# Kernel tuning notes

Measured on AMD Instinct MI355X. Metric: run time of the kernel, lower is better.

Reference implementation:

```python
import jax, jax.numpy as jnp
import numpy as np

N_EMBD = 1024
N_HEAD = 16
HEAD_DIM = N_EMBD // N_HEAD

def setup_inputs() -> dict:
    key = jax.random.key(0)
    ks = jax.random.split(key, 5)
    B, T, C = 2, 2048, N_EMBD
    s = 1.0 / np.sqrt(C)
    x = jax.random.normal(ks[0], (B, T, C), dtype=jnp.float32)
    W_qkv = jax.random.normal(ks[1], (C, 3 * C), dtype=jnp.float32) * s
    b_qkv = jax.random.normal(ks[2], (3 * C,), dtype=jnp.float32) * 0.02
    W_o = jax.random.normal(ks[3], (C, C), dtype=jnp.float32) * s
    b_o = jax.random.normal(ks[4], (C,), dtype=jnp.float32) * 0.02
    return {"x": x, "W_qkv": W_qkv, "b_qkv": b_qkv, "W_o": W_o, "b_o": b_o}

def reference(x, W_qkv, b_qkv, W_o, b_o):
    B, T, C = x.shape
    H, D = N_HEAD, HEAD_DIM
    scale = 1.0 / np.sqrt(D)
    qkv = jnp.einsum('btc,cf->btf', x, W_qkv) + b_qkv  # [B,T,3C]
    q, k, v = jnp.split(qkv, 3, axis=-1)
    # [B,H,T,D]
    q = q.reshape(B, T, H, D).transpose(0, 2, 1, 3)
    k = k.reshape(B, T, H, D).transpose(0, 2, 1, 3)
    v = v.reshape(B, T, H, D).transpose(0, 2, 1, 3)
    att = jnp.einsum('bhqd,bhkd->bhqk', q, k) * scale  # [B,H,T,T]
    causal = jnp.tril(jnp.ones((T, T), dtype=bool))
    att = jnp.where(causal[None, None], att, -jnp.inf)
    att = jax.nn.softmax(att, axis=-1)
    y = jnp.einsum('bhqk,bhkd->bhqd', att, v)  # [B,H,T,D]
    y = y.transpose(0, 2, 1, 3).reshape(B, T, C)
    return jnp.einsum('btc,cf->btf', y, W_o) + b_o
```

## Files before the change

kernel.cpp:

```cpp
#include <hip/hip_runtime.h>
#include <hip/hip_bf16.h>

#define TT 2048
#define BB 2
#define CC 1024
#define NH 16
#define HD 64

typedef __attribute__((ext_vector_type(8))) short short8;
typedef __attribute__((ext_vector_type(4))) short short4b;
typedef __attribute__((ext_vector_type(4))) float f32x4;

typedef unsigned int __attribute__((address_space(1))) ui_gas;
typedef unsigned int __attribute__((address_space(3))) ui_las;

#if __has_builtin(__builtin_amdgcn_mfma_f32_16x16x16bf16_1k)
#define PV16 1
#define VSS 4
#else
#define PV16 0
#define VSS 8
#endif

__device__ __forceinline__ float us2f(unsigned short u) {
    union { unsigned int i; float f; } v; v.i = ((unsigned int)u) << 16; return v.f;
}
__device__ __forceinline__ unsigned short f2us(float f) {
    union { float f; unsigned int i; } v; v.f = f;
    unsigned int i = v.i;
    unsigned int lsb = (i >> 16) & 1u;
    i += 0x7fffu + lsb;
    return (unsigned short)(i >> 16);
}
__device__ __forceinline__ unsigned int pack2_trunc(float a, float b) {
    union { float f; unsigned int u; } x, y; x.f = a; y.f = b;
    return (y.u & 0xffff0000u) | (x.u >> 16);
}

__device__ __forceinline__ void gl_lds16(const unsigned short* g, unsigned short* l) {
    __builtin_amdgcn_global_load_lds((const ui_gas*)g, (ui_las*)l, 16, 0, 0);
}

__device__ __forceinline__ float4 load4(const void* p, size_t i, int isbf) {
    if (isbf) {
        ushort4 u = *reinterpret_cast<const ushort4*>((const unsigned short*)p + i);
        return make_float4(us2f(u.x), us2f(u.y), us2f(u.z), us2f(u.w));
    } else {
        return *reinterpret_cast<const float4*>((const float*)p + i);
    }
}
__device__ __forceinline__ float load1(const void* p, size_t i, int isbf) {
    return isbf ? us2f(((const unsigned short*)p)[i]) : ((const float*)p)[i];
}

__global__ __launch_bounds__(256) void prep_kernel(
    const void* __restrict__ x, const void* __restrict__ Wqkv, const void* __restrict__ Wo,
    const void* __restrict__ bqkv, const void* __restrict__ bo,
    unsigned short* __restrict__ xb, unsigned short* __restrict__ Wqkvt,
    unsigned short* __restrict__ Wot, int* __restrict__ flags)
{
    __shared__ float Ls[64 * 65];
    __shared__ int sh_isbf;
    const int t = threadIdx.x;
    const int bid = blockIdx.x;

    const void* src;
    int mode, sub;
    if (bid < 2048)      { mode = 0; sub = bid;        src = x; }
    else if (bid < 2816) { mode = 1; sub = bid - 2048; src = Wqkv; }
    else                 { mode = 2; sub = bid - 2816; src = Wo; }

    if (bid == 0 && t < 64) {
        const void* ps[5] = {x, Wqkv, bqkv, Wo, bo};
        for (int k = 0; k < 5; ++k) {
            const unsigned short* u = (const unsigned short*)ps[k];
            int bad = 0;
            #pragma unroll
            for (int j = 0; j < 4; ++j) {
                float v = us2f(u[t * 4 + j]);
                if (!(fabsf(v) < 1e4f)) bad = 1;
            }
            unsigned long long m = __ballot(bad != 0);
            if (t == 0) flags[k] = (__popcll(m) < 4) ? 1 : 0;
        }
    }
    if (t < 64) {
        const unsigned short* u = (const unsigned short*)src;
        int bad = 0;
        #pragma unroll
        for (int j = 0; j < 4; ++j) {
            float v = us2f(u[t * 4 + j]);
            if (!(fabsf(v) < 1e4f)) bad = 1;
        }
        unsigned long long m = __ballot(bad != 0);
        if (t == 0) sh_isbf = (__popcll(m) < 4) ? 1 : 0;
    }
    __syncthreads();
    const int isbf = sh_isbf;

    if (mode == 0) {
        const size_t i = ((size_t)sub * 256 + t) * 8;
        float4 a = load4(src, i, isbf);
        float4 b = load4(src, i + 4, isbf);
        alignas(16) unsigned short pk[8];
        pk[0] = f2us(a.x); pk[1] = f2us(a.y); pk[2] = f2us(a.z); pk[3] = f2us(a.w);
        pk[4] = f2us(b.x); pk[5] = f2us(b.y); pk[6] = f2us(b.z); pk[7] = f2us(b.w);
        *reinterpret_cast<uint4*>(xb + i) = *reinterpret_cast<const uint4*>(pk);
        return;
    }

    int N, Krows, n0, k0;
    unsigned short* dst;
    if (mode == 1) { N = 3 * CC; Krows = CC; dst = Wqkvt; n0 = (sub % 48) * 64; k0 = (sub / 48) * 64; }
    else           { N = CC;     Krows = CC; dst = Wot;   n0 = (sub % 16) * 64; k0 = (sub / 16) * 64; }
    {
        const int r = t >> 2, cq = (t & 3) << 4;
        #pragma unroll
        for (int i = 0; i < 4; ++i) {
            float4 v = load4(src, (size_t)(k0 + r) * N + n0 + cq + i * 4, isbf);
            Ls[r * 65 + cq + i * 4 + 0] = v.x;
            Ls[r * 65 + cq + i * 4 + 1] = v.y;
            Ls[r * 65 + cq + i * 4 + 2] = v.z;
            Ls[r * 65 + cq + i * 4 + 3] = v.w;
        }
    }
    __syncthreads();
    {
        const int c = t & 63, kg = (t >> 6) * 16;
        alignas(16) unsigned short pk[16];
        #pragma unroll
        for (int i = 0; i < 16; ++i) pk[i] = f2us(Ls[(kg + i) * 65 + c]);
        unsigned short* d = dst + (size_t)(n0 + c) * Krows + k0 + kg;
        *reinterpret_cast<uint4*>(d + 0) = *reinterpret_cast<const uint4*>(&pk[0]);
        *reinterpret_cast<uint4*>(d + 8) = *reinterpret_cast<const uint4*>(&pk[8]);
    }
}

template<int WM, int WN, int NWM, int NWN>
__global__ __launch_bounds__(256) void gemm_mfma(
    const unsigned short* __restrict__ A,
    const unsigned short* __restrict__ Bt,
    const void* __restrict__ bias, void* __restrict__ C,
    unsigned short* __restrict__ Vt,
    int M, int N, int K,
    const int* __restrict__ flags, int biasfi, int cfi)
{
    constexpr int BM = WM * 16 * NWM, BN = WN * 16 * NWN;
    constexpr int ASL = BM / 16, BSL = BN / 16;

    const int bias_bf = (biasfi >= 0) ? flags[biasfi] : 0;
    const int c_bf    = (cfi >= 0) ? flags[cfi] : ((cfi == -2) ? 1 : 0);

    __shared__ __align__(16) unsigned short Asl[2][ASL * 2 * 512];
    __shared__ __align__(16) unsigned short Bsl[2][BSL * 2 * 512];

    const int tid = threadIdx.x;
    const int l  = tid & 63;
    const int w  = tid >> 6;
    const int wm = w / NWN, wn = w % NWN;
    const int bm = blockIdx.y * BM, bn = blockIdx.x * BN;
    const int lm = l & 15;
    const int lk = (l >> 4) * 8;

    f32x4 acc[WM][WN];
    #pragma unroll
    for (int i = 0; i < WM; ++i)
        #pragma unroll
        for (int j = 0; j < WN; ++j) acc[i][j] = (f32x4){0.f, 0.f, 0.f, 0.f};

    auto stage = [&](int bb, int k0) {
        #pragma unroll
        for (int s = 0; s < ASL / 4; ++s) {
            const int r = w * (ASL / 4) + s;
            #pragma unroll
            for (int kh = 0; kh < 2; ++kh)
                gl_lds16(A + (size_t)(bm + r * 16 + lm) * K + k0 + kh * 32 + lk,
                         &Asl[bb][(r * 2 + kh) * 512]);
        }
        #pragma unroll
        for (int s = 0; s < BSL / 4; ++s) {
            const int r = w * (BSL / 4) + s;
            #pragma unroll
            for (int kh = 0; kh < 2; ++kh)
                gl_lds16(Bt + (size_t)(bn + r * 16 + lm) * K + k0 + kh * 32 + lk,
                         &Bsl[bb][(r * 2 + kh) * 512]);
        }
    };

    auto compute = [&](int bb) {
        #pragma unroll
        for (int kh = 0; kh < 2; ++kh) {
            short8 af[WM], bf[WN];
            #pragma unroll
            for (int i = 0; i < WM; ++i)
                af[i] = *reinterpret_cast<const short8*>(&Asl[bb][((WM * wm + i) * 2 + kh) * 512 + l * 8]);
            #pragma unroll
            for (int j = 0; j < WN; ++j)
                bf[j] = *reinterpret_cast<const short8*>(&Bsl[bb][((WN * wn + j) * 2 + kh) * 512 + l * 8]);
            #pragma unroll
            for (int i = 0; i < WM; ++i)
                #pragma unroll
                for (int j = 0; j < WN; ++j)
                    acc[i][j] = __builtin_amdgcn_mfma_f32_16x16x32_bf16(af[i], bf[j], acc[i][j], 0, 0, 0);
        }
    };

    stage(0, 0);
    __syncthreads();
    const int nt = K >> 6;
    for (int t = 0; t < nt; ++t) {
        if (t + 1 < nt) stage((t + 1) & 1, (t + 1) << 6);
        compute(t & 1);
        __syncthreads();
    }

    const int quad = l >> 4;
    float bv[WN];
    #pragma unroll
    for (int j = 0; j < WN; ++j) bv[j] = load1(bias, bn + (WN * wn + j) * 16 + lm, bias_bf);

    #pragma unroll
    for (int i = 0; i < WM; ++i) {
        #pragma unroll
        for (int r = 0; r < 4; ++r) {
            const int row = bm + (WM * wm + i) * 16 + quad * 4 + r;
            #pragma unroll
            for (int j = 0; j < WN; ++j) {
                const int col = bn + (WN * wn + j) * 16 + lm;
                const float val = acc[i][j][r] + bv[j];
                if (c_bf) {
                    const unsigned short us = f2us(val);
                    ((unsigned short*)C)[(size_t)row * N + col] = us;
                    if (Vt != nullptr && col >= 2 * CC) {
                        const int cc2 = col - 2 * CC;
                        const int h = cc2 >> 6, d = cc2 & 63;
                        const int bq = row / TT, tk = row % TT;
                        Vt[((size_t)(bq * NH + h) * HD + d) * TT + tk] = us;
                    }
                } else {
                    ((float*)C)[(size_t)row * N + col] = val;
                }
            }
        }
    }
}

__global__ __launch_bounds__(256) void attn_mfma(
    const unsigned short* __restrict__ qkv,
    const unsigned short* __restrict__ Vt,
    unsigned short* __restrict__ y)
{
    __shared__ __align__(16) unsigned short Ksh[2][8 * 512];
    __shared__ __align__(16) unsigned short Vsh[2][1039 * VSS];

    const int tid = threadIdx.x;
    const int l   = tid & 63;
    const int w   = tid >> 6;
    const int quad = l >> 4;
    const int col  = l & 15;

    const int n  = blockIdx.x;
    const int g  = n >> 3;
    const int bh = (n & 7) * 4 + (g & 3);
    const int i  = g >> 2;
    const int tA = i, tB = 31 - i;
    const int b  = bh >> 4, h = bh & 15;

#if !PV16
    {
        unsigned short* vflat = &Vsh[0][0];
        for (int ss = tid; ss < 1039 * 2; ss += 256)
            *(uint2*)(&vflat[ss * 8 + 4]) = make_uint2(0u, 0u);
    }
#endif

    const float QSCALE = 0.18033688f;
    short8 qfA[2], qfB[2];
    #pragma unroll
    for (int t2 = 0; t2 < 2; ++t2) {
        const int qt = t2 ? tB : tA;
        short8* qf = t2 ? qfB : qfA;
        const int token = qt * 64 + w * 16 + col;
        const unsigned short* qrow = qkv + (size_t)(b * TT + token) * 3 * CC + h * HD;
        #pragma unroll
        for (int ks = 0; ks < 2; ++ks) {
            ushort4 u0 = *(const ushort4*)(qrow + ks * 32 + quad * 8);
            ushort4 u1 = *(const ushort4*)(qrow + ks * 32 + quad * 8 + 4);
            alignas(16) unsigned short pk[8];
            pk[0] = f2us(us2f(u0.x) * QSCALE);
            pk[1] = f2us(us2f(u0.y) * QSCALE);
            pk[2] = f2us(us2f(u0.z) * QSCALE);
            pk[3] = f2us(us2f(u0.w) * QSCALE);
            pk[4] = f2us(us2f(u1.x) * QSCALE);
            pk[5] = f2us(us2f(u1.y) * QSCALE);
            pk[6] = f2us(us2f(u1.z) * QSCALE);
            pk[7] = f2us(us2f(u1.w) * QSCALE);
            qf[ks] = *(const short8*)pk;
        }
    }

    f32x4 oA[4], oB[4];
    #pragma unroll
    for (int nb = 0; nb < 4; ++nb) {
        oA[nb] = (f32x4){0.f, 0.f, 0.f, 0.f};
        oB[nb] = (f32x4){0.f, 0.f, 0.f, 0.f};
    }
    float lAc = 0.f, lBc = 0.f;

    const unsigned short* kbase = qkv + (size_t)b * TT * 3 * CC + CC + h * HD;
    const unsigned short* vbase = Vt + (size_t)bh * HD * TT;

    const int vd = tid >> 2, vg0 = (tid & 3) * 4;

    uint4 rk[2], rv[2];
    auto issue_loads = [&](int kt) {
        const unsigned short* ksrc = kbase + (size_t)(kt * 64 + l) * 3 * CC;
        #pragma unroll
        for (int c2 = 0; c2 < 2; ++c2) {
            const int c = 2 * w + c2;
            rk[c2] = *(const uint4*)(ksrc + c * 8);
        }
        const unsigned short* vsrc = vbase + (size_t)vd * TT + kt * 64 + vg0 * 4;
        rv[0] = *(const uint4*)(vsrc + 0);
        rv[1] = *(const uint4*)(vsrc + 8);
    };
    auto write_lds = [&](int bb) {
        #pragma unroll
        for (int c2 = 0; c2 < 2; ++c2) {
            const int c = 2 * w + c2;
            const int ks = c >> 2, q = c & 3;
            const int slot = ((quad * 2 + ks) * 64 + q * 16 + col) * 8;
            *(uint4*)(&Ksh[bb][slot]) = rk[c2];
        }
        *(uint2*)(&Vsh[bb][((vg0 + 0) * 65 + vd) * VSS]) = make_uint2(rv[0].x, rv[0].y);
        *(uint2*)(&Vsh[bb][((vg0 + 1) * 65 + vd) * VSS]) = make_uint2(rv[0].z, rv[0].w);
        *(uint2*)(&Vsh[bb][((vg0 + 2) * 65 + vd) * VSS]) = make_uint2(rv[1].x, rv[1].y);
        *(uint2*)(&Vsh[bb][((vg0 + 3) * 65 + vd) * VSS]) = make_uint2(rv[1].z, rv[1].w);
    };

    auto step = [&](const short8* qf, f32x4* o, float& l_i, bool diag, int bb) {
        f32x4 st[4];
        __builtin_amdgcn_s_setprio(1);
        #pragma unroll
        for (int nb = 0; nb < 4; ++nb) {
            f32x4 acc = {0.f, 0.f, 0.f, 0.f};
            #pragma unroll
            for (int ks = 0; ks < 2; ++ks) {
                short8 kf = *(const short8*)(&Ksh[bb][((nb * 2 + ks) * 64 + l) * 8]);
                acc = __builtin_amdgcn_mfma_f32_16x16x32_bf16(kf, qf[ks], acc, 0, 0, 0);
            }
            st[nb] = acc;
        }
        __builtin_amdgcn_s_setprio(0);
        float pv[4][4];
        float rs = 0.f;
        #pragma unroll
        for (int nb = 0; nb < 4; ++nb)
            #pragma unroll
            for (int r = 0; r < 4; ++r) {
                float v = st[nb][r];
                if (diag && (nb * 16 + quad * 4 + r > w * 16 + col)) v = -3e38f;
                float p = __builtin_exp2f(v);
                pv[nb][r] = p;
                rs += p;
            }
        rs += __shfl_xor(rs, 16);
        rs += __shfl_xor(rs, 32);
        l_i += rs;
#if PV16
        short4b pf[4];
        #pragma unroll
        for (int nbk = 0; nbk < 4; ++nbk) {
            union { short4b s; unsigned int u[2]; } pk;
            pk.u[0] = pack2_trunc(pv[nbk][0], pv[nbk][1]);
            pk.u[1] = pack2_trunc(pv[nbk][2], pv[nbk][3]);
            pf[nbk] = pk.s;
        }
        __builtin_amdgcn_s_setprio(1);
        #pragma unroll
        for (int nbd = 0; nbd < 4; ++nbd)
            #pragma unroll
            for (int nbk = 0; nbk < 4; ++nbk) {
                short4b vf = *(const short4b*)(&Vsh[bb][((nbk * 4 + quad) * 65 + nbd * 16 + col) * VSS]);
                o[nbd] = __builtin_amdgcn_mfma_f32_16x16x16bf16_1k(pf[nbk], vf, o[nbd], 0, 0, 0);
            }
        __builtin_amdgcn_s_setprio(0);
#else
        short8 pf[4];
        #pragma unroll
        for (int nbk = 0; nbk < 4; ++nbk) {
            union { short8 s; unsigned int u[4]; } pk;
            pk.u[0] = pack2_trunc(pv[nbk][0], pv[nbk][1]);
            pk.u[1] = pack2_trunc(pv[nbk][2], pv[nbk][3]);
            pk.u[2] = 0u; pk.u[3] = 0u;
            pf[nbk] = pk.s;
        }
        __builtin_amdgcn_s_setprio(1);
        #pragma unroll
        for (int nbd = 0; nbd < 4; ++nbd)
            #pragma unroll
            for (int nbk = 0; nbk < 4; ++nbk) {
                short8 vf = *(const short8*)(&Vsh[bb][((nbk * 4 + quad) * 65 + nbd * 16 + col) * VSS]);
                o[nbd] = __builtin_amdgcn_mfma_f32_16x16x32_bf16(pf[nbk], vf, o[nbd], 0, 0, 0);
            }
        __builtin_amdgcn_s_setprio(0);
#endif
    };

    issue_loads(0);
    write_lds(0);
    __syncthreads();
    for (int kt = 0; kt <= tB; ++kt) {
        const int cur = kt & 1;
        if (kt < tB) issue_loads(kt + 1);
        step(qfB, oB, lBc, kt == tB, cur);
        if (kt <= tA) step(qfA, oA, lAc, kt == tA, cur);
        if (kt < tB) write_lds(cur ^ 1);
        __syncthreads();
    }

    #pragma unroll
    for (int t2 = 0; t2 < 2; ++t2) {
        const int qt = t2 ? tB : tA;
        f32x4* o = t2 ? oB : oA;
        const float inv = 1.f / (t2 ? lBc : lAc);
        float invr[4];
        #pragma unroll
        for (int r = 0; r < 4; ++r) invr[r] = __shfl(inv, quad * 4 + r);
        #pragma unroll
        for (int nb = 0; nb < 4; ++nb)
            #pragma unroll
            for (int r = 0; r < 4; ++r) {
                int token = qt * 64 + w * 16 + quad * 4 + r;
                y[(size_t)(b * TT + token) * CC + h * HD + nb * 16 + col] = f2us(o[nb][r] * invr[r]);
            }
    }
}

extern "C" void kernel_launch(void* const* d_in, const int* in_sizes, int n_in,
                              void* d_out, int out_size, void* d_ws, size_t ws_size,
                              hipStream_t stream) {
    const int M = BB * TT;

    char* ws = (char*)d_ws;
    int*            flags = (int*)ws;                         ws += 256;
    unsigned short* xb    = (unsigned short*)ws;              ws += (size_t)M * CC * 2;
    unsigned short* Wqkvt = (unsigned short*)ws;              ws += (size_t)3 * CC * CC * 2;
    unsigned short* Wot   = (unsigned short*)ws;              ws += (size_t)CC * CC * 2;
    unsigned short* qkv   = (unsigned short*)ws;              ws += (size_t)M * 3 * CC * 2;
    unsigned short* Vt    = (unsigned short*)ws;              ws += (size_t)BB * NH * HD * TT * 2;
    unsigned short* y     = (unsigned short*)ws;

    prep_kernel<<<3072, 256, 0, stream>>>(d_in[0], d_in[1], d_in[3], d_in[2], d_in[4],
                                          xb, Wqkvt, Wot, flags);

    gemm_mfma<4, 4, 2, 2><<<dim3(3 * CC / 128, M / 128), 256, 0, stream>>>(
        xb, Wqkvt, d_in[2], qkv, Vt, M, 3 * CC, CC, flags, 2, -2);

    attn_mfma<<<512, 256, 0, stream>>>(qkv, Vt, y);

    gemm_mfma<2, 4, 4, 1><<<dim3(CC / 64, M / 128), 256, 0, stream>>>(
        y, Wot, d_in[4], d_out, nullptr, M, CC, CC, flags, 4, 0);
}
```

Measured before the change: 249.3 us.

## Replace LDS-staged GEMMs with register-direct global loads and XCD-aware block swizzle

Both projection GEMMs drop the shared-memory double-buffered staging and barriers. Each wave now loads its MFMA fragments straight from global memory into registers, double-buffered across 32-wide K steps with the K loop fully unrolled. Block indices are remapped so blocks landing on the same XCD cover neighbouring tiles, which is meant to improve L2 reuse, and the QKV GEMM tile shape changes to 256x64. This removes LDS traffic and sync overhead, but each wave now reads its own A/B data with no sharing inside the block, so global and L2 traffic rises and register pressure grows.

```diff
diff --git a/kernel.cpp b/kernel.cpp
--- a/kernel.cpp
+++ b/kernel.cpp
@@ -35,10 +35,6 @@
 __device__ __forceinline__ unsigned int pack2_trunc(float a, float b) {
     union { float f; unsigned int u; } x, y; x.f = a; y.f = b;
     return (y.u & 0xffff0000u) | (x.u >> 16);
-}
-
-__device__ __forceinline__ void gl_lds16(const unsigned short* g, unsigned short* l) {
-    __builtin_amdgcn_global_load_lds((const ui_gas*)g, (ui_las*)l, 16, 0, 0);
 }
 
 __device__ __forceinline__ float4 load4(const void* p, size_t i, int isbf) {
@@ -136,106 +132,105 @@
     }
 }
 
-template<int WM, int WN, int NWM, int NWN>
-__global__ __launch_bounds__(256) void gemm_mfma(
+template<int WM, int WN, int KC, int SWZ, bool VTE>
+__global__ __launch_bounds__(256) void gemm_reg(
     const unsigned short* __restrict__ A,
     const unsigned short* __restrict__ Bt,
     const void* __restrict__ bias, void* __restrict__ C,
     unsigned short* __restrict__ Vt,
-    int M, int N, int K,
+    int M, int N,
     const int* __restrict__ flags, int biasfi, int cfi)
 {
-    constexpr int BM = WM * 16 * NWM, BN = WN * 16 * NWN;
-    constexpr int ASL = BM / 16, BSL = BN / 16;
+    constexpr int HS = KC / 32;
+    const int tid = threadIdx.x;
+    const int l   = tid & 63;
+    const int w   = tid >> 6;
+    const int lm  = l & 15;
+    const int lk  = (l >> 4) * 8;
+    const int quad = l >> 4;
+
+    int bx, by;
+    if constexpr (SWZ == 1) {
+        const int lin = blockIdx.y * 48 + blockIdx.x;
+        const int xcd = lin & 7, loc = lin >> 3;
+        bx = (xcd & 3) * 12 + loc % 12;
+        by = (xcd >> 2) * 8 + loc / 12;
+    } else if constexpr (SWZ == 2) {
+        const int lin = blockIdx.y * 16 + blockIdx.x;
+        const int xcd = lin & 7, loc = lin >> 3;
+        bx = (xcd & 1) * 8 + (loc & 7);
+        by = (xcd >> 1) * 8 + (loc >> 3);
+    } else {
+        bx = blockIdx.x; by = blockIdx.y;
+    }
+
+    const int wrow = (by * 4 + w) * (WM * 16);
+    const int wcol = bx * (WN * 16);
+
+    const unsigned short* pa[WM];
+    const unsigned short* pb[WN];
+    #pragma unroll
+    for (int i = 0; i < WM; ++i) pa[i] = A  + (size_t)(wrow + i * 16 + lm) * KC + lk;
+    #pragma unroll
+    for (int j = 0; j < WN; ++j) pb[j] = Bt + (size_t)(wcol + j * 16 + lm) * KC + lk;
+
+    f32x4 acc[WM][WN];
+    #pragma unroll
+    for (int i = 0; i < WM; ++i)
+        #pragma unroll
+        for (int j = 0; j < WN; ++j) acc[i][j] = (f32x4){0.f, 0.f, 0.f, 0.f};
+
+    short8 fa0[WM], fb0[WN], fa1[WM], fb1[WN];
+
+    auto loadh = [&](short8* fa, short8* fb, int off) {
+        #pragma unroll
+        for (int i = 0; i < WM; ++i) fa[i] = *reinterpret_cast<const short8*>(pa[i] + off);
+        #pragma unroll
+        for (int j = 0; j < WN; ++j) fb[j] = *reinterpret_cast<const short8*>(pb[j] + off);
+    };
+    auto mfmah = [&](short8* fa, short8* fb) {
+        #pragma unroll
+        for (int i = 0; i < WM; ++i)
+            #pragma unroll
+            for (int j = 0; j < WN; ++j)
+                acc[i][j] = __builtin_amdgcn_mfma_f32_16x16x32_bf16(fa[i], fb[j], acc[i][j], 0, 0, 0);
+    };
+
+    loadh(fa0, fb0, 0);
+    #pragma unroll
+    for (int hs = 0; hs < HS; ++hs) {
+        if ((hs & 1) == 0) {
+            if (hs + 1 < HS) loadh(fa1, fb1, (hs + 1) * 32);
+            mfmah(fa0, fb0);
+        } else {
+            if (hs + 1 < HS) loadh(fa0, fb0, (hs + 1) * 32);
+            mfmah(fa1, fb1);
+        }
+    }
 
     const int bias_bf = (biasfi >= 0) ? flags[biasfi] : 0;
     const int c_bf    = (cfi >= 0) ? flags[cfi] : ((cfi == -2) ? 1 : 0);
-
-    __shared__ __align__(16) unsigned short Asl[2][ASL * 2 * 512];
-    __shared__ __align__(16) unsigned short Bsl[2][BSL * 2 * 512];
-
-    const int tid = threadIdx.x;
-    const int l  = tid & 63;
-    const int w  = tid >> 6;
-    const int wm = w / NWN, wn = w % NWN;
-    const int bm = blockIdx.y * BM, bn = blockIdx.x * BN;
-    const int lm = l & 15;
-    const int lk = (l >> 4) * 8;
-
-    f32x4 acc[WM][WN];
-    #pragma unroll
-    for (int i = 0; i < WM; ++i)
-        #pragma unroll
-        for (int j = 0; j < WN; ++j) acc[i][j] = (f32x4){0.f, 0.f, 0.f, 0.f};
-
-    auto stage = [&](int bb, int k0) {
-        #pragma unroll
-        for (int s = 0; s < ASL / 4; ++s) {
-            const int r = w * (ASL / 4) + s;
-            #pragma unroll
-            for (int kh = 0; kh < 2; ++kh)
-                gl_lds16(A + (size_t)(bm + r * 16 + lm) * K + k0 + kh * 32 + lk,
-                         &Asl[bb][(r * 2 + kh) * 512]);
-        }
-        #pragma unroll
-        for (int s = 0; s < BSL / 4; ++s) {
-            const int r = w * (BSL / 4) + s;
-            #pragma unroll
-            for (int kh = 0; kh < 2; ++kh)
-                gl_lds16(Bt + (size_t)(bn + r * 16 + lm) * K + k0 + kh * 32 + lk,
-                         &Bsl[bb][(r * 2 + kh) * 512]);
-        }
-    };
-
-    auto compute = [&](int bb) {
-        #pragma unroll
-        for (int kh = 0; kh < 2; ++kh) {
-            short8 af[WM], bf[WN];
-            #pragma unroll
-            for (int i = 0; i < WM; ++i)
-                af[i] = *reinterpret_cast<const short8*>(&Asl[bb][((WM * wm + i) * 2 + kh) * 512 + l * 8]);
-            #pragma unroll
-            for (int j = 0; j < WN; ++j)
-                bf[j] = *reinterpret_cast<const short8*>(&Bsl[bb][((WN * wn + j) * 2 + kh) * 512 + l * 8]);
-            #pragma unroll
-            for (int i = 0; i < WM; ++i)
-                #pragma unroll
-                for (int j = 0; j < WN; ++j)
-                    acc[i][j] = __builtin_amdgcn_mfma_f32_16x16x32_bf16(af[i], bf[j], acc[i][j], 0, 0, 0);
-        }
-    };
-
-    stage(0, 0);
-    __syncthreads();
-    const int nt = K >> 6;
-    for (int t = 0; t < nt; ++t) {
-        if (t + 1 < nt) stage((t + 1) & 1, (t + 1) << 6);
-        compute(t & 1);
-        __syncthreads();
-    }
-
-    const int quad = l >> 4;
     float bv[WN];
     #pragma unroll
-    for (int j = 0; j < WN; ++j) bv[j] = load1(bias, bn + (WN * wn + j) * 16 + lm, bias_bf);
+    for (int j = 0; j < WN; ++j) bv[j] = load1(bias, wcol + j * 16 + lm, bias_bf);
 
     #pragma unroll
     for (int i = 0; i < WM; ++i) {
         #pragma unroll
         for (int r = 0; r < 4; ++r) {
-            const int row = bm + (WM * wm + i) * 16 + quad * 4 + r;
+            const int row = wrow + i * 16 + quad * 4 + r;
             #pragma unroll
             for (int j = 0; j < WN; ++j) {
-                const int col = bn + (WN * wn + j) * 16 + lm;
+                const int col = wcol + j * 16 + lm;
                 const float val = acc[i][j][r] + bv[j];
                 if (c_bf) {
                     const unsigned short us = f2us(val);
                     ((unsigned short*)C)[(size_t)row * N + col] = us;
-                    if (Vt != nullptr && col >= 2 * CC) {
+                    if (VTE && col >= 2 * CC) {
                         const int cc2 = col - 2 * CC;
-                        const int h = cc2 >> 6, d = cc2 & 63;
-                        const int bq = row / TT, tk = row % TT;
-                        Vt[((size_t)(bq * NH + h) * HD + d) * TT + tk] = us;
+                        const int hh = cc2 >> 6, dd = cc2 & 63;
+                        const int bq = row >> 11, tk = row & (TT - 1);
+                        Vt[((size_t)(bq * NH + hh) * HD + dd) * TT + tk] = us;
                     }
                 } else {
                     ((float*)C)[(size_t)row * N + col] = val;
@@ -454,11 +449,11 @@
     prep_kernel<<<3072, 256, 0, stream>>>(d_in[0], d_in[1], d_in[3], d_in[2], d_in[4],
                                           xb, Wqkvt, Wot, flags);
 
-    gemm_mfma<4, 4, 2, 2><<<dim3(3 * CC / 128, M / 128), 256, 0, stream>>>(
-        xb, Wqkvt, d_in[2], qkv, Vt, M, 3 * CC, CC, flags, 2, -2);
+    gemm_reg<4, 4, CC, 1, true><<<dim3(3 * CC / 64, M / 256), 256, 0, stream>>>(
+        xb, Wqkvt, d_in[2], qkv, Vt, M, 3 * CC, flags, 2, -2);
 
     attn_mfma<<<512, 256, 0, stream>>>(qkv, Vt, y);
 
-    gemm_mfma<2, 4, 4, 1><<<dim3(CC / 64, M / 128), 256, 0, stream>>>(
-        y, Wot, d_in[4], d_out, nullptr, M, CC, CC, flags, 4, 0);
-}
+    gemm_reg<2, 4, CC, 2, false><<<dim3(CC / 64, M / 128), 256, 0, stream>>>(
+        y, Wot, d_in[4], d_out, nullptr, M, CC, flags, 4, 0);
+}
```

Measured after the change: 299.8 us. 1.2x slower.

## Triple-buffer GEMM K-loop, swizzle blocks per XCD, stage V transpose through LDS

Applied to the files above, without the earlier changes.

The GEMM mainloop now uses K-steps of 32 with a three-stage LDS ring. Explicit vmcnt waits and raw barriers let two tiles be in flight, so global loads overlap with MFMA work. Block indices are remapped so neighbouring tiles land on the same XCD for better L2 reuse. The scattered V-transpose stores are replaced by an LDS staging pass that writes coalesced 16-byte rows. The output projection is retiled to 64x64 blocks for more parallelism. The cost is more barriers per K, and the swizzle hard-codes the grid sizes.

```diff
diff --git a/kernel.cpp b/kernel.cpp
--- a/kernel.cpp
+++ b/kernel.cpp
@@ -136,7 +136,7 @@
     }
 }
 
-template<int WM, int WN, int NWM, int NWN>
+template<int WM, int WN, int NWM, int NWN, int SWZ, bool VTE>
 __global__ __launch_bounds__(256) void gemm_mfma(
     const unsigned short* __restrict__ A,
     const unsigned short* __restrict__ Bt,
@@ -147,20 +147,34 @@
 {
     constexpr int BM = WM * 16 * NWM, BN = WN * 16 * NWN;
     constexpr int ASL = BM / 16, BSL = BN / 16;
-
-    const int bias_bf = (biasfi >= 0) ? flags[biasfi] : 0;
-    const int c_bf    = (cfi >= 0) ? flags[cfi] : ((cfi == -2) ? 1 : 0);
-
-    __shared__ __align__(16) unsigned short Asl[2][ASL * 2 * 512];
-    __shared__ __align__(16) unsigned short Bsl[2][BSL * 2 * 512];
+    constexpr int TOT = ASL + BSL;
+    constexpr int PW  = TOT / 4;
+
+    __shared__ __align__(16) unsigned short SH[3][TOT * 512];
 
     const int tid = threadIdx.x;
     const int l  = tid & 63;
     const int w  = tid >> 6;
     const int wm = w / NWN, wn = w % NWN;
-    const int bm = blockIdx.y * BM, bn = blockIdx.x * BN;
     const int lm = l & 15;
     const int lk = (l >> 4) * 8;
+    const int quad = l >> 4;
+
+    int bx, by;
+    if constexpr (SWZ == 1) {
+        const int lin = blockIdx.y * 24 + blockIdx.x;
+        const int xcd = lin & 7, loc = lin >> 3;
+        bx = (xcd & 1) * 12 + loc % 12;
+        by = (xcd >> 1) * 8 + loc / 12;
+    } else if constexpr (SWZ == 2) {
+        const int lin = blockIdx.y * 16 + blockIdx.x;
+        const int xcd = lin & 7, loc = lin >> 3;
+        bx = (xcd & 1) * 8 + (loc & 7);
+        by = (xcd >> 1) * 16 + (loc >> 3);
+    } else {
+        bx = blockIdx.x; by = blockIdx.y;
+    }
+    const int bm = by * BM, bn = bx * BN;
 
     f32x4 acc[WM][WN];
     #pragma unroll
@@ -170,77 +184,96 @@
 
     auto stage = [&](int bb, int k0) {
         #pragma unroll
-        for (int s = 0; s < ASL / 4; ++s) {
-            const int r = w * (ASL / 4) + s;
-            #pragma unroll
-            for (int kh = 0; kh < 2; ++kh)
-                gl_lds16(A + (size_t)(bm + r * 16 + lm) * K + k0 + kh * 32 + lk,
-                         &Asl[bb][(r * 2 + kh) * 512]);
-        }
-        #pragma unroll
-        for (int s = 0; s < BSL / 4; ++s) {
-            const int r = w * (BSL / 4) + s;
-            #pragma unroll
-            for (int kh = 0; kh < 2; ++kh)
-                gl_lds16(Bt + (size_t)(bn + r * 16 + lm) * K + k0 + kh * 32 + lk,
-                         &Bsl[bb][(r * 2 + kh) * 512]);
+        for (int s = 0; s < PW; ++s) {
+            const int slab = w * PW + s;
+            const unsigned short* src;
+            if (slab < ASL) src = A  + (size_t)(bm + slab * 16 + lm) * K + k0 + lk;
+            else            src = Bt + (size_t)(bn + (slab - ASL) * 16 + lm) * K + k0 + lk;
+            gl_lds16(src, &SH[bb][slab * 512]);
         }
     };
 
     auto compute = [&](int bb) {
-        #pragma unroll
-        for (int kh = 0; kh < 2; ++kh) {
-            short8 af[WM], bf[WN];
-            #pragma unroll
-            for (int i = 0; i < WM; ++i)
-                af[i] = *reinterpret_cast<const short8*>(&Asl[bb][((WM * wm + i) * 2 + kh) * 512 + l * 8]);
+        short8 af[WM], bf[WN];
+        #pragma unroll
+        for (int i = 0; i < WM; ++i)
+            af[i] = *reinterpret_cast<const short8*>(&SH[bb][(wm * WM + i) * 512 + l * 8]);
+        #pragma unroll
+        for (int j = 0; j < WN; ++j)
+            bf[j] = *reinterpret_cast<const short8*>(&SH[bb][(ASL + wn * WN + j) * 512 + l * 8]);
+        #pragma unroll
+        for (int i = 0; i < WM; ++i)
             #pragma unroll
             for (int j = 0; j < WN; ++j)
-                bf[j] = *reinterpret_cast<const short8*>(&Bsl[bb][((WN * wn + j) * 2 + kh) * 512 + l * 8]);
-            #pragma unroll
-            for (int i = 0; i < WM; ++i)
-                #pragma unroll
-                for (int j = 0; j < WN; ++j)
-                    acc[i][j] = __builtin_amdgcn_mfma_f32_16x16x32_bf16(af[i], bf[j], acc[i][j], 0, 0, 0);
-        }
+                acc[i][j] = __builtin_amdgcn_mfma_f32_16x16x32_bf16(af[i], bf[j], acc[i][j], 0, 0, 0);
     };
 
+    const int nt = K >> 5;
     stage(0, 0);
-    __syncthreads();
-    const int nt = K >> 6;
+    stage(1, 32);
+    asm volatile("s_waitcnt vmcnt(%0)" :: "n"(PW) : "memory");
+    __builtin_amdgcn_sched_barrier(0);
+    __builtin_amdgcn_s_barrier();
+
     for (int t = 0; t < nt; ++t) {
-        if (t + 1 < nt) stage((t + 1) & 1, (t + 1) << 6);
-        compute(t & 1);
-        __syncthreads();
-    }
-
-    const int quad = l >> 4;
+        if (t + 2 < nt) stage((t + 2) % 3, (t + 2) << 5);
+        compute(t % 3);
+        if (t + 2 < nt) {
+            asm volatile("s_waitcnt vmcnt(%0)" :: "n"(PW) : "memory");
+        } else {
+            asm volatile("s_waitcnt vmcnt(0)" ::: "memory");
+        }
+        __builtin_amdgcn_sched_barrier(0);
+        __builtin_amdgcn_s_barrier();
+    }
+
+    const int bias_bf = (biasfi >= 0) ? flags[biasfi] : 0;
+    const int c_bf    = (cfi >= 0) ? flags[cfi] : ((cfi == -2) ? 1 : 0);
     float bv[WN];
     #pragma unroll
     for (int j = 0; j < WN; ++j) bv[j] = load1(bias, bn + (WN * wn + j) * 16 + lm, bias_bf);
 
+    constexpr int TS = BM + 8;
+    unsigned short* FL = &SH[0][0];
+    const bool vblk = VTE && (bn >= 2 * CC);
+
     #pragma unroll
     for (int i = 0; i < WM; ++i) {
         #pragma unroll
         for (int r = 0; r < 4; ++r) {
-            const int row = bm + (WM * wm + i) * 16 + quad * 4 + r;
+            const int rl = (WM * wm + i) * 16 + quad * 4 + r;
+            const int row = bm + rl;
             #pragma unroll
             for (int j = 0; j < WN; ++j) {
-                const int col = bn + (WN * wn + j) * 16 + lm;
+                const int cl2 = (WN * wn + j) * 16 + lm;
+                const int col = bn + cl2;
                 const float val = acc[i][j][r] + bv[j];
                 if (c_bf) {
                     const unsigned short us = f2us(val);
                     ((unsigned short*)C)[(size_t)row * N + col] = us;
-                    if (Vt != nullptr && col >= 2 * CC) {
-                        const int cc2 = col - 2 * CC;
-                        const int h = cc2 >> 6, d = cc2 & 63;
-                        const int bq = row / TT, tk = row % TT;
-                        Vt[((size_t)(bq * NH + h) * HD + d) * TT + tk] = us;
-                    }
+                    if (vblk) FL[cl2 * TS + rl] = us;
                 } else {
                     ((float*)C)[(size_t)row * N + col] = val;
                 }
             }
+        }
+    }
+
+    if constexpr (VTE) {
+        static_assert(!VTE || (BM == 128 && BN % 64 == 0), "VTE geometry");
+        static_assert(!VTE || (BN * (BM + 8) <= 3 * TOT * 512), "VTE LDS overlay");
+        if (vblk) {
+            __syncthreads();
+            const int cl = tid >> 1, rq = tid & 1;
+            const int cc2 = bn - 2 * CC + cl;
+            const int hh = cc2 >> 6, dd = cc2 & 63;
+            const int bq = bm >> 11;
+            const int tk = (bm & (TT - 1)) + rq * 64;
+            unsigned short* dst = Vt + ((size_t)(bq * NH + hh) * HD + dd) * TT + tk;
+            const unsigned short* srcp = &FL[cl * TS + rq * 64];
+            #pragma unroll
+            for (int k = 0; k < 8; ++k)
+                *(uint4*)(dst + k * 8) = *(const uint4*)(srcp + k * 8);
         }
     }
 }
@@ -454,11 +487,11 @@
     prep_kernel<<<3072, 256, 0, stream>>>(d_in[0], d_in[1], d_in[3], d_in[2], d_in[4],
                                           xb, Wqkvt, Wot, flags);
 
-    gemm_mfma<4, 4, 2, 2><<<dim3(3 * CC / 128, M / 128), 256, 0, stream>>>(
+    gemm_mfma<4, 4, 2, 2, 1, true><<<dim3(3 * CC / 128, M / 128), 256, 0, stream>>>(
         xb, Wqkvt, d_in[2], qkv, Vt, M, 3 * CC, CC, flags, 2, -2);
 
     attn_mfma<<<512, 256, 0, stream>>>(qkv, Vt, y);
 
-    gemm_mfma<2, 4, 4, 1><<<dim3(CC / 64, M / 128), 256, 0, stream>>>(
+    gemm_mfma<2, 2, 2, 2, 2, false><<<dim3(CC / 64, M / 64), 256, 0, stream>>>(
         y, Wot, d_in[4], d_out, nullptr, M, CC, CC, flags, 4, 0);
 }
```

New measurement: 231.3 us. -7.2%, faster.
